# Performance work log

Hardware: AMD Instinct MI355X
Metric: run time of the kernel (lower is better)

The kernel has to match this reference:

```python
import jax, jax.numpy as jnp
import numpy as np
import math

B, S, D, H, DFF = 4, 2048, 1024, 16, 4096
DK = D // H
EPS = 1e-5

def setup_inputs() -> dict:
    key = jax.random.key(0)
    ks = jax.random.split(key, 16)
    s_d = 1.0 / math.sqrt(D)
    s_ff = 1.0 / math.sqrt(DFF)
    return {
        "x": jax.random.normal(ks[0], (B, S, D), jnp.float32),
        "wq": jax.random.uniform(ks[1], (D, D), jnp.float32, -s_d, s_d),
        "bq": jnp.zeros((D,), jnp.float32),
        "wk": jax.random.uniform(ks[2], (D, D), jnp.float32, -s_d, s_d),
        "bk": jnp.zeros((D,), jnp.float32),
        "wv": jax.random.uniform(ks[3], (D, D), jnp.float32, -s_d, s_d),
        "bv": jnp.zeros((D,), jnp.float32),
        "wo": jax.random.uniform(ks[4], (D, D), jnp.float32, -s_d, s_d),
        "bo": jnp.zeros((D,), jnp.float32),
        "w1": jax.random.uniform(ks[5], (DFF, D), jnp.float32, -s_d, s_d),
        "b1": jnp.zeros((DFF,), jnp.float32),
        "w2": jax.random.uniform(ks[6], (D, DFF), jnp.float32, -s_ff, s_ff),
        "b2": jnp.zeros((D,), jnp.float32),
        "ln1_g": jnp.ones((D,), jnp.float32),
        "ln1_b": jnp.zeros((D,), jnp.float32),
        "ln2_g": jnp.ones((D,), jnp.float32),
        "ln2_b": jnp.zeros((D,), jnp.float32),
    }

def _layernorm(x, g, b):
    mu = jnp.mean(x, axis=-1, keepdims=True)
    var = jnp.mean(jnp.square(x - mu), axis=-1, keepdims=True)
    return (x - mu) * jax.lax.rsqrt(var + EPS) * g + b

def reference(x, wq, bq, wk, bk, wv, bv, wo, bo, w1, b1, w2, b2, ln1_g, ln1_b, ln2_g, ln2_b):
    # Multi-head self-attention (dropout in eval mode -> identity).
    Q = (x @ wq.T + bq).reshape(B, S, H, DK).transpose(0, 2, 1, 3)  # (B,H,S,DK)
    K = (x @ wk.T + bk).reshape(B, S, H, DK).transpose(0, 2, 1, 3)
    V = (x @ wv.T + bv).reshape(B, S, H, DK).transpose(0, 2, 1, 3)
    scores = jnp.einsum('bhqd,bhkd->bhqk', Q, K) / math.sqrt(DK)  # (B,H,S,S)
    attn = jax.nn.softmax(scores, axis=-1)
    ctx = jnp.einsum('bhqk,bhkd->bhqd', attn, V)
    ctx = ctx.transpose(0, 2, 1, 3).reshape(B, S, D)
    attn_out = ctx @ wo.T + bo
    # SkipConnection: x + norm(sublayer)  (post-applied LayerNorm on sublayer output)
    x = x + _layernorm(attn_out, ln1_g, ln1_b)
    # FFN
    ff = jax.nn.relu(x @ w1.T + b1) @ w2.T + b2
    return x + _layernorm(ff, ln2_g, ln2_b)
```

## Files before the change

kernel.cpp:

```cpp
#include <hip/hip_runtime.h>
#include <hip/hip_bf16.h>
#include <stdint.h>


#define DI __device__ __forceinline__

typedef __attribute__((ext_vector_type(4))) float f32x4;
typedef __attribute__((ext_vector_type(16))) float f32x16;
typedef __attribute__((ext_vector_type(8))) short bf16x8;
typedef __attribute__((ext_vector_type(4))) short s16x4;

#define B_ 4
#define S_ 2048
#define D_ 1024
#define H_ 16
#define DK_ 64
#define DFF_ 4096
#define M_ 8192

DI float bf2f(short s) {
  union { unsigned u; float f; } v;
  v.u = ((unsigned)(unsigned short)s) << 16;
  return v.f;
}
DI short f2bf(float f) {
  union { float f; unsigned u; } v;
  v.f = f;
  unsigned r = v.u + 0x7FFFu + ((v.u >> 16) & 1u);
  return (short)(r >> 16);
}
DI unsigned pkbf(float lo, float hi) {
  unsigned r;
  asm("v_cvt_pk_bf16_f32 %0, %1, %2" : "=v"(r) : "v"(lo), "v"(hi));
  return r;
}
DI void plswap(unsigned& a, unsigned& b) {
  asm volatile("v_permlane32_swap_b32 %0, %1" : "+v"(a), "+v"(b));
}
DI float ex2(float x) {
  float r;
  asm("v_exp_f32 %0, %1" : "=v"(r) : "v"(x));
  return r;
}
DI float max3(float a, float b, float c) {
  float r;
  asm("v_max3_f32 %0, %1, %2, %3" : "=v"(r) : "v"(a), "v"(b), "v"(c));
  return r;
}

__global__ __launch_bounds__(256) void cvt_kernel(const float* __restrict__ in,
                                                  short* __restrict__ out, int n) {
  long i = ((long)blockIdx.x * blockDim.x + threadIdx.x) * 8;
  if (i >= n) return;
  f32x4 a = *(const f32x4*)(in + i);
  f32x4 b = *(const f32x4*)(in + i + 4);
  bf16x8 r;
  r[0] = f2bf(a[0]); r[1] = f2bf(a[1]); r[2] = f2bf(a[2]); r[3] = f2bf(a[3]);
  r[4] = f2bf(b[0]); r[5] = f2bf(b[1]); r[6] = f2bf(b[2]); r[7] = f2bf(b[3]);
  *(bf16x8*)(out + i) = r;
}

DI void gl_lds16(const void* g, void* l) {
  __builtin_amdgcn_global_load_lds(
      (const __attribute__((address_space(1))) unsigned int*)g,
      (__attribute__((address_space(3))) unsigned int*)l, 16, 0, 0);
}

#define VMCNT(N) asm volatile("s_waitcnt vmcnt(" #N ")" ::: "memory")
#define LGKM0                                          \
  asm volatile("s_waitcnt lgkmcnt(0)" ::: "memory");   \
  __builtin_amdgcn_sched_barrier(0)
#define BAR __builtin_amdgcn_s_barrier()
#define PRIO1 __builtin_amdgcn_s_setprio(1)
#define PRIO0 __builtin_amdgcn_s_setprio(0)

DI bf16x8 ldf(const short* base, int row, int kk, int lk) {
  return *(const bf16x8*)(base + row * 64 + (((4 * kk + lk) ^ (row & 7)) << 3));
}

template <int BN, int MODE>
__global__ __launch_bounds__(512, 2)
void gemm8p(const short* __restrict__ A, const short* __restrict__ Bm,
            const float* __restrict__ bias0, const float* __restrict__ bias1,
            const float* __restrict__ bias2, short* __restrict__ C,
            int M, int N, int K,
            short* __restrict__ Qo, short* __restrict__ Ko, short* __restrict__ Vo) {
  constexpr int BH = BN / 128;
  constexpr int MQ = (BN == 256 ? 4 : 2);
  constexpr int NQ = 2;
  constexpr int MF = 2 * MQ;
  constexpr int NFr = 4;
  constexpr int WM = (BN == 256 ? 128 : 64);
  constexpr int WN = 64;

  __shared__ short As[2 * 2 * 8192];
  __shared__ short Bs[2 * BH * 8192];

  const int t = threadIdx.x, w = t >> 6, l = t & 63;
  const int wm = (BN == 256 ? (w >> 2) : (w >> 1));
  const int wn = (BN == 256 ? (w & 3) : (w & 1));
  const int lr = l & 15, lk = l >> 4;
  const int ah = (BN == 256 ? wm : (wm >> 1));
  const int ab = (BN == 256 ? 0 : (wm & 1) * 64);
  const int bh = (BN == 256 ? (wn >> 1) : 0);
  const int bb = (BN == 256 ? (wn & 1) * 64 : wn * 64);

  const int gx = gridDim.x, gy = gridDim.y;
  const int orig = blockIdx.y * gx + blockIdx.x;
  const int xcd = orig & 7, k7 = orig >> 3;
  const int rw = gx >> 1, rh = gy >> 2;
  const int row0 = ((xcd >> 1) * rh + k7 / rw) * 256;
  const int col0 = ((xcd & 1) * rw + k7 % rw) * BN;

  const int NT = K >> 6;

  const int rl0 = t >> 3;
  const int csw = ((t & 7) ^ (rl0 & 7)) << 3;
  const short* Abase = A + (long)row0 * K;
  const short* Bbase = Bm + (long)col0 * K;

  auto stA = [&](int b, int kt, int h) {
    short* dst = As + ((b * 2 + h) << 13);
    const short* s = Abase + (long)(h * 128 + rl0) * K + (kt << 6) + csw;
    gl_lds16(s, dst + t * 8);
    gl_lds16(s + (long)64 * K, dst + (t + 512) * 8);
  };
  auto stB = [&](int b, int kt, int h) {
    short* dst = Bs + ((b * BH + h) << 13);
    const short* s = Bbase + (long)(h * 128 + rl0) * K + (kt << 6) + csw;
    gl_lds16(s, dst + t * 8);
    gl_lds16(s + (long)64 * K, dst + (t + 512) * 8);
  };

  f32x4 acc[MF][NFr] = {};

  stA(0, 0, 0); stA(0, 0, 1);
  stB(0, 0, 0); if (BH == 2) stB(0, 0, 1);
  stB(1, 1, 0); if (BH == 2) stB(1, 1, 1);
  stA(1, 1, 0);
  if (BH == 2) { VMCNT(6); } else { VMCNT(4); }
  BAR;

  for (int u = 0; u < NT; ++u) {
    const int rb = u & 1, ob = rb ^ 1;
    const short* aw = As + ((rb * 2 + ah) << 13);
    const short* bw = Bs + ((rb * BH + bh) << 13);
    const bool m1 = (u + 1 < NT), m2 = (u + 2 < NT);
    bf16x8 a0[MQ][2], a1[MQ][2], b0[NQ][2], b1[NQ][2];

#pragma unroll
    for (int m = 0; m < MQ; ++m) {
      const int r = ab + m * 16 + lr;
      a0[m][0] = ldf(aw, r, 0, lk); a0[m][1] = ldf(aw, r, 1, lk);
    }
#pragma unroll
    for (int n = 0; n < NQ; ++n) {
      const int r = bb + n * 16 + lr;
      b0[n][0] = ldf(bw, r, 0, lk); b0[n][1] = ldf(bw, r, 1, lk);
    }
    if (m1) stA(ob, u + 1, 1);
    BAR; LGKM0; PRIO1;
#pragma unroll
    for (int m = 0; m < MQ; ++m)
#pragma unroll
      for (int n = 0; n < NQ; ++n)
#pragma unroll
        for (int kk = 0; kk < 2; ++kk)
          acc[m][n] = __builtin_amdgcn_mfma_f32_16x16x32_bf16(
              a0[m][kk], b0[n][kk], acc[m][n], 0, 0, 0);
    PRIO0; BAR;

#pragma unroll
    for (int n = 0; n < NQ; ++n) {
      const int r = bb + (NQ + n) * 16 + lr;
      b1[n][0] = ldf(bw, r, 0, lk); b1[n][1] = ldf(bw, r, 1, lk);
    }
    BAR; LGKM0; PRIO1;
#pragma unroll
    for (int m = 0; m < MQ; ++m)
#pragma unroll
      for (int n = 0; n < NQ; ++n)
#pragma unroll
        for (int kk = 0; kk < 2; ++kk)
          acc[m][NQ + n] = __builtin_amdgcn_mfma_f32_16x16x32_bf16(
              a0[m][kk], b1[n][kk], acc[m][NQ + n], 0, 0, 0);
    PRIO0; BAR;

#pragma unroll
    for (int m = 0; m < MQ; ++m) {
      const int r = ab + (MQ + m) * 16 + lr;
      a1[m][0] = ldf(aw, r, 0, lk); a1[m][1] = ldf(aw, r, 1, lk);
    }
    if (m2) stB(rb, u + 2, 0);
    BAR; LGKM0; PRIO1;
#pragma unroll
    for (int m = 0; m < MQ; ++m)
#pragma unroll
      for (int n = 0; n < NQ; ++n)
#pragma unroll
        for (int kk = 0; kk < 2; ++kk)
          acc[MQ + m][NQ + n] = __builtin_amdgcn_mfma_f32_16x16x32_bf16(
              a1[m][kk], b1[n][kk], acc[MQ + m][NQ + n], 0, 0, 0);
    PRIO0; BAR;

    if (m2) { if (BH == 2) stB(rb, u + 2, 1); stA(rb, u + 2, 0); }
    BAR; PRIO1;
#pragma unroll
    for (int m = 0; m < MQ; ++m)
#pragma unroll
      for (int n = 0; n < NQ; ++n)
#pragma unroll
        for (int kk = 0; kk < 2; ++kk)
          acc[MQ + m][n] = __builtin_amdgcn_mfma_f32_16x16x32_bf16(
              a1[m][kk], b0[n][kk], acc[MQ + m][n], 0, 0, 0);
    PRIO0;
    if (m2) {
      if (BH == 2) { VMCNT(6); } else { VMCNT(4); }
    } else {
      VMCNT(0);
    }
    BAR;
  }

  if (MODE == 2) {
    const int which = col0 >> 10;
#pragma unroll
    for (int m = 0; m < MF; ++m) {
#pragma unroll
      for (int n = 0; n < NFr; ++n) {
        const int r0e = row0 + wm * WM + m * 16 + lk * 4;
        const int c = col0 + wn * WN + n * 16 + lr;
        const int cc = c & 1023;
        const int h = cc >> 6, dk = cc & 63;
        const int bbx = r0e >> 11, s = r0e & 2047;
        if (which == 2) {
          const float bias = bias2[cc];
          s16x4 v4;
#pragma unroll
          for (int j = 0; j < 4; ++j) v4[j] = f2bf(acc[m][n][j] + bias);
          *(s16x4*)(Vo + ((long)((bbx * H_ + h) * DK_ + dk)) * S_ + s) = v4;
        } else {
          const float bias = (which == 0 ? bias0[cc] : bias1[cc]);
          const float sc = (which == 0 ? 0.1803368801f : 1.0f);
          short* dst = (which == 0 ? Qo : Ko);
#pragma unroll
          for (int j = 0; j < 4; ++j)
            dst[(((long)(bbx * H_ + h) * S_) + s + j) * DK_ + dk] =
                f2bf((acc[m][n][j] + bias) * sc);
        }
      }
    }
  } else {
#pragma unroll
    for (int m = 0; m < MF; ++m) {
#pragma unroll
      for (int n = 0; n < NFr; ++n) {
#pragma unroll
        for (int j = 0; j < 4; ++j) {
          const int r = row0 + wm * WM + m * 16 + lk * 4 + j;
          const int c = col0 + wn * WN + n * 16 + lr;
          float v = acc[m][n][j] + bias0[c];
          if (MODE == 1) v = fmaxf(v, 0.0f);
          C[(long)r * N + c] = f2bf(v);
        }
      }
    }
  }
}

__global__ __launch_bounds__(512, 4)
void attn_kernel(const short* __restrict__ Q, const short* __restrict__ K,
                 const short* __restrict__ Vt, short* __restrict__ ctx) {
  __shared__ short Ks[2 * 4096];
  __shared__ short Vs[2 * 4096];
  const int t = threadIdx.x, w = t >> 6, l = t & 63;
  const int q31 = l & 31, hi = l >> 5;

  const int orig = blockIdx.y * gridDim.x + blockIdx.x;
  const int xcd = orig & 7, k7 = orig >> 3;
  const int bh = xcd * 8 + (k7 >> 3);
  const int q0 = (k7 & 7) * 256 + w * 32;
  const long base = (long)bh * S_ * DK_;

  bf16x8 qf[4];
  {
    const short* qp = Q + base + (long)(q0 + q31) * DK_ + hi * 8;
#pragma unroll
    for (int ks = 0; ks < 4; ++ks) qf[ks] = *(const bf16x8*)(qp + ks * 16);
  }

  bf16x8 ones;
#pragma unroll
  for (int i = 0; i < 8; ++i) ones[i] = (short)0x3F80;

  f32x16 oa[2] = {};
  f32x16 lacc = {};
  float mrun = -1e30f;

  const int trow = t >> 3;
  const int tcol = (((t & 7) ^ (trow & 7)) << 3);
  const short* Ksrc = K + base + (long)trow * DK_ + tcol;
  const short* Vsrc = Vt + base + (long)trow * S_ + tcol;

  auto stg = [&](int tile, int slot) {
    const int kb = slot * 4096;
    const int kvn = tile * 64;
    gl_lds16(Ksrc + (long)kvn * DK_, &Ks[kb + t * 8]);
    gl_lds16(Vsrc + kvn, &Vs[kb + t * 8]);
  };

  stg(0, 0);

  for (int tt = 0; tt < 32; ++tt) {
    VMCNT(0);
    BAR;
    if (tt + 1 < 32) stg(tt + 1, (tt + 1) & 1);
    const int cb = (tt & 1) * 4096;

    f32x16 sacc[2] = {};
#pragma unroll
    for (int m = 0; m < 2; ++m) {
      const int row = m * 32 + q31;
      const int sw = row & 7;
#pragma unroll
      for (int ks = 0; ks < 4; ++ks) {
        bf16x8 kf = *(const bf16x8*)&Ks[cb + row * 64 + (((2 * ks + hi) ^ sw) << 3)];
        sacc[m] = __builtin_amdgcn_mfma_f32_32x32x16_bf16(kf, qf[ks], sacc[m], 0, 0, 0);
      }
    }

    float mx[8];
#pragma unroll
    for (int r = 0; r < 8; ++r)
      mx[r] = fmaxf(max3(sacc[0][r], sacc[0][r + 8], sacc[1][r]), sacc[1][r + 8]);
    float ma = max3(mx[0], mx[1], mx[2]);
    float mb = max3(mx[3], mx[4], mx[5]);
    float tm = fmaxf(max3(mx[6], mx[7], ma), mb);
    tm = fmaxf(tm, __shfl_xor(tm, 32, 64));

    if (!__all(tm <= mrun + 8.0f)) {
      const float mnew = fmaxf(mrun, tm);
      const float fac = ex2(mrun - mnew);
#pragma unroll
      for (int r = 0; r < 16; ++r) lacc[r] *= fac;
#pragma unroll
      for (int m = 0; m < 2; ++m)
#pragma unroll
        for (int r = 0; r < 16; ++r) oa[m][r] *= fac;
      mrun = mnew;
    }

#pragma unroll
    for (int m = 0; m < 2; ++m)
#pragma unroll
      for (int r = 0; r < 16; ++r) sacc[m][r] = ex2(sacc[m][r] - mrun);

    bf16x8 pf[4];
#pragma unroll
    for (int m = 0; m < 2; ++m)
#pragma unroll
      for (int sb = 0; sb < 2; ++sb) {
        unsigned p0 = pkbf(sacc[m][8 * sb + 0], sacc[m][8 * sb + 1]);
        unsigned p1 = pkbf(sacc[m][8 * sb + 2], sacc[m][8 * sb + 3]);
        unsigned p2 = pkbf(sacc[m][8 * sb + 4], sacc[m][8 * sb + 5]);
        unsigned p3 = pkbf(sacc[m][8 * sb + 6], sacc[m][8 * sb + 7]);
        plswap(p0, p2);
        plswap(p1, p3);
        union { unsigned u[4]; bf16x8 v; } fb;
        fb.u[0] = p0; fb.u[1] = p1; fb.u[2] = p2; fb.u[3] = p3;
        pf[2 * m + sb] = fb.v;
      }

#pragma unroll
    for (int s = 0; s < 4; ++s) {
      lacc = __builtin_amdgcn_mfma_f32_32x32x16_bf16(ones, pf[s], lacc, 0, 0, 0);
#pragma unroll
      for (int mt = 0; mt < 2; ++mt) {
        const int row = mt * 32 + q31;
        const int sw = row & 7;
        bf16x8 vf = *(const bf16x8*)&Vs[cb + row * 64 + (((2 * s + hi) ^ sw) << 3)];
        oa[mt] = __builtin_amdgcn_mfma_f32_32x32x16_bf16(vf, pf[s], oa[mt], 0, 0, 0);
      }
    }
  }

  const int bb2 = bh >> 4, h = bh & 15;
  const float rl = 1.0f / lacc[0];
  short* crow = ctx + ((long)(bb2 * S_ + q0 + q31)) * D_ + h * 64 + 4 * hi;
#pragma unroll
  for (int mt = 0; mt < 2; ++mt)
#pragma unroll
    for (int g = 0; g < 4; ++g) {
      s16x4 v4;
#pragma unroll
      for (int i = 0; i < 4; ++i) v4[i] = f2bf(oa[mt][4 * g + i] * rl);
      *(s16x4*)(crow + mt * 32 + g * 8) = v4;
    }
}

template <int RES_BF16, int OUT_BF16>
__global__ __launch_bounds__(256)
void add_ln(const void* __restrict__ resv, const short* __restrict__ a,
            const float* __restrict__ gam, const float* __restrict__ bet,
            void* __restrict__ outv) {
  const int row = blockIdx.x, t = threadIdx.x;
  const int w = t >> 6, l = t & 63;
  const long roff = (long)row * D_;
  const int c = t * 4;
  s16x4 av = *(const s16x4*)(a + roff + c);
  float v0 = bf2f(av[0]), v1 = bf2f(av[1]), v2 = bf2f(av[2]), v3 = bf2f(av[3]);
  float s = v0 + v1 + v2 + v3;
#pragma unroll
  for (int mask = 1; mask < 64; mask <<= 1) s += __shfl_xor(s, mask, 64);
  __shared__ float r1[4], r2[4];
  if (l == 0) r1[w] = s;
  __syncthreads();
  float mu = (r1[0] + r1[1] + r1[2] + r1[3]) * (1.0f / D_);
  float d0 = v0 - mu, d1 = v1 - mu, d2 = v2 - mu, d3 = v3 - mu;
  float sq = d0 * d0 + d1 * d1 + d2 * d2 + d3 * d3;
#pragma unroll
  for (int mask = 1; mask < 64; mask <<= 1) sq += __shfl_xor(sq, mask, 64);
  if (l == 0) r2[w] = sq;
  __syncthreads();
  float var = (r2[0] + r2[1] + r2[2] + r2[3]) * (1.0f / D_);
  float rs = rsqrtf(var + 1e-5f);
  float res0, res1, res2, res3;
  if (RES_BF16) {
    s16x4 rv = *(const s16x4*)((const short*)resv + roff + c);
    res0 = bf2f(rv[0]); res1 = bf2f(rv[1]); res2 = bf2f(rv[2]); res3 = bf2f(rv[3]);
  } else {
    f32x4 rv = *(const f32x4*)((const float*)resv + roff + c);
    res0 = rv[0]; res1 = rv[1]; res2 = rv[2]; res3 = rv[3];
  }
  float o0 = res0 + d0 * rs * gam[c + 0] + bet[c + 0];
  float o1 = res1 + d1 * rs * gam[c + 1] + bet[c + 1];
  float o2 = res2 + d2 * rs * gam[c + 2] + bet[c + 2];
  float o3 = res3 + d3 * rs * gam[c + 3] + bet[c + 3];
  if (OUT_BF16) {
    s16x4 ov;
    ov[0] = f2bf(o0); ov[1] = f2bf(o1); ov[2] = f2bf(o2); ov[3] = f2bf(o3);
    *(s16x4*)((short*)outv + roff + c) = ov;
  } else {
    f32x4 ov;
    ov[0] = o0; ov[1] = o1; ov[2] = o2; ov[3] = o3;
    *(f32x4*)((float*)outv + roff + c) = ov;
  }
}

extern "C" void kernel_launch(void* const* d_in, const int* in_sizes, int n_in,
                              void* d_out, int out_size, void* d_ws, size_t ws_size,
                              hipStream_t stream) {
  (void)in_sizes; (void)n_in; (void)out_size; (void)ws_size;
  const float* x   = (const float*)d_in[0];
  const float* wq  = (const float*)d_in[1];
  const float* bq  = (const float*)d_in[2];
  const float* wk  = (const float*)d_in[3];
  const float* bk  = (const float*)d_in[4];
  const float* wv  = (const float*)d_in[5];
  const float* bv  = (const float*)d_in[6];
  const float* wo  = (const float*)d_in[7];
  const float* bo  = (const float*)d_in[8];
  const float* w1  = (const float*)d_in[9];
  const float* b1  = (const float*)d_in[10];
  const float* w2  = (const float*)d_in[11];
  const float* b2  = (const float*)d_in[12];
  const float* g1  = (const float*)d_in[13];
  const float* be1 = (const float*)d_in[14];
  const float* g2  = (const float*)d_in[15];
  const float* be2 = (const float*)d_in[16];

  char* ws = (char*)d_ws;
  const long MB = 1 << 20;
  short* xb    = (short*)(ws + 0 * MB);
  short* wqkvb = (short*)(ws + 16 * MB);
  short* wob   = (short*)(ws + 22 * MB);
  short* w1b   = (short*)(ws + 24 * MB);
  short* w2b   = (short*)(ws + 32 * MB);
  short* Qb    = (short*)(ws + 40 * MB);
  short* Kb    = (short*)(ws + 56 * MB);
  short* Vtb   = (short*)(ws + 72 * MB);
  short* ctxb  = (short*)(ws + 88 * MB);
  short* aout  = (short*)(ws + 40 * MB);
  short* x1b   = (short*)(ws + 56 * MB);
  short* hid   = (short*)(ws + 88 * MB);
  short* ffb   = (short*)(ws + 72 * MB);

  auto cvt = [&](const float* in, short* out, long n) {
    cvt_kernel<<<dim3((unsigned)((n / 8 + 255) / 256)), dim3(256), 0, stream>>>(in, out, (int)n);
  };
  cvt(x, xb, (long)M_ * D_);
  cvt(wq, wqkvb + 0L * D_ * D_, (long)D_ * D_);
  cvt(wk, wqkvb + 1L * D_ * D_, (long)D_ * D_);
  cvt(wv, wqkvb + 2L * D_ * D_, (long)D_ * D_);
  cvt(wo, wob, (long)D_ * D_);
  cvt(w1, w1b, (long)DFF_ * D_);
  cvt(w2, w2b, (long)D_ * DFF_);

  gemm8p<256, 2><<<dim3(3072 / 256, M_ / 256), 512, 0, stream>>>(
      xb, wqkvb, bq, bk, bv, nullptr, M_, 3072, D_, Qb, Kb, Vtb);

  attn_kernel<<<dim3(S_ / 256, B_ * H_), 512, 0, stream>>>(Qb, Kb, Vtb, ctxb);

  gemm8p<128, 0><<<dim3(D_ / 128, M_ / 256), 512, 0, stream>>>(
      ctxb, wob, bo, nullptr, nullptr, aout, M_, D_, D_, nullptr, nullptr, nullptr);

  add_ln<0, 1><<<dim3(M_), 256, 0, stream>>>(x, aout, g1, be1, x1b);

  gemm8p<256, 1><<<dim3(DFF_ / 256, M_ / 256), 512, 0, stream>>>(
      x1b, w1b, b1, nullptr, nullptr, hid, M_, DFF_, D_, nullptr, nullptr, nullptr);
  gemm8p<128, 0><<<dim3(D_ / 128, M_ / 256), 512, 0, stream>>>(
      hid, w2b, b2, nullptr, nullptr, ffb, M_, D_, DFF_, nullptr, nullptr, nullptr);

  add_ln<1, 0><<<dim3(M_), 256, 0, stream>>>(x1b, ffb, g2, be2, d_out);
}
```

Baseline: 389.6 us.

## Add dedicated simpler pipelined main loop for BN=128 GEMM tiles

Splits the GEMM main loop by tile width. The BN=256 path keeps the existing four-phase interleaved schedule. The BN=128 path gets its own loop: it loads all fragments at once, issues the global-to-LDS prefetch for tile u+2 right after one barrier, then runs a single 4x4 MFMA block. This drops the extra barriers and phase splitting for the narrower tile, with the risk of less overlap between LDS reads and MFMA issue.

```diff
diff --git a/kernel.cpp b/kernel.cpp
--- a/kernel.cpp
+++ b/kernel.cpp
@@ -134,92 +134,128 @@
 
   f32x4 acc[MF][NFr] = {};
 
-  stA(0, 0, 0); stA(0, 0, 1);
-  stB(0, 0, 0); if (BH == 2) stB(0, 0, 1);
-  stB(1, 1, 0); if (BH == 2) stB(1, 1, 1);
-  stA(1, 1, 0);
-  if (BH == 2) { VMCNT(6); } else { VMCNT(4); }
-  BAR;
-
-  for (int u = 0; u < NT; ++u) {
-    const int rb = u & 1, ob = rb ^ 1;
-    const short* aw = As + ((rb * 2 + ah) << 13);
-    const short* bw = Bs + ((rb * BH + bh) << 13);
-    const bool m1 = (u + 1 < NT), m2 = (u + 2 < NT);
-    bf16x8 a0[MQ][2], a1[MQ][2], b0[NQ][2], b1[NQ][2];
-
-#pragma unroll
-    for (int m = 0; m < MQ; ++m) {
-      const int r = ab + m * 16 + lr;
-      a0[m][0] = ldf(aw, r, 0, lk); a0[m][1] = ldf(aw, r, 1, lk);
-    }
-#pragma unroll
-    for (int n = 0; n < NQ; ++n) {
-      const int r = bb + n * 16 + lr;
-      b0[n][0] = ldf(bw, r, 0, lk); b0[n][1] = ldf(bw, r, 1, lk);
-    }
-    if (m1) stA(ob, u + 1, 1);
-    BAR; LGKM0; PRIO1;
-#pragma unroll
-    for (int m = 0; m < MQ; ++m)
-#pragma unroll
-      for (int n = 0; n < NQ; ++n)
-#pragma unroll
-        for (int kk = 0; kk < 2; ++kk)
-          acc[m][n] = __builtin_amdgcn_mfma_f32_16x16x32_bf16(
-              a0[m][kk], b0[n][kk], acc[m][n], 0, 0, 0);
-    PRIO0; BAR;
-
-#pragma unroll
-    for (int n = 0; n < NQ; ++n) {
-      const int r = bb + (NQ + n) * 16 + lr;
-      b1[n][0] = ldf(bw, r, 0, lk); b1[n][1] = ldf(bw, r, 1, lk);
-    }
-    BAR; LGKM0; PRIO1;
-#pragma unroll
-    for (int m = 0; m < MQ; ++m)
-#pragma unroll
-      for (int n = 0; n < NQ; ++n)
-#pragma unroll
-        for (int kk = 0; kk < 2; ++kk)
-          acc[m][NQ + n] = __builtin_amdgcn_mfma_f32_16x16x32_bf16(
-              a0[m][kk], b1[n][kk], acc[m][NQ + n], 0, 0, 0);
-    PRIO0; BAR;
-
-#pragma unroll
-    for (int m = 0; m < MQ; ++m) {
-      const int r = ab + (MQ + m) * 16 + lr;
-      a1[m][0] = ldf(aw, r, 0, lk); a1[m][1] = ldf(aw, r, 1, lk);
-    }
-    if (m2) stB(rb, u + 2, 0);
-    BAR; LGKM0; PRIO1;
-#pragma unroll
-    for (int m = 0; m < MQ; ++m)
-#pragma unroll
-      for (int n = 0; n < NQ; ++n)
-#pragma unroll
-        for (int kk = 0; kk < 2; ++kk)
-          acc[MQ + m][NQ + n] = __builtin_amdgcn_mfma_f32_16x16x32_bf16(
-              a1[m][kk], b1[n][kk], acc[MQ + m][NQ + n], 0, 0, 0);
-    PRIO0; BAR;
-
-    if (m2) { if (BH == 2) stB(rb, u + 2, 1); stA(rb, u + 2, 0); }
-    BAR; PRIO1;
-#pragma unroll
-    for (int m = 0; m < MQ; ++m)
-#pragma unroll
-      for (int n = 0; n < NQ; ++n)
-#pragma unroll
-        for (int kk = 0; kk < 2; ++kk)
-          acc[MQ + m][n] = __builtin_amdgcn_mfma_f32_16x16x32_bf16(
-              a1[m][kk], b0[n][kk], acc[MQ + m][n], 0, 0, 0);
-    PRIO0;
-    if (m2) {
-      if (BH == 2) { VMCNT(6); } else { VMCNT(4); }
-    } else {
-      VMCNT(0);
-    }
+  if constexpr (BN == 256) {
+    stA(0, 0, 0); stA(0, 0, 1);
+    stB(0, 0, 0); stB(0, 0, 1);
+    stB(1, 1, 0); stB(1, 1, 1);
+    stA(1, 1, 0);
+    VMCNT(6);
     BAR;
+
+    for (int u = 0; u < NT; ++u) {
+      const int rb = u & 1, ob = rb ^ 1;
+      const short* aw = As + ((rb * 2 + ah) << 13);
+      const short* bw = Bs + ((rb * BH + bh) << 13);
+      const bool m1 = (u + 1 < NT), m2 = (u + 2 < NT);
+      bf16x8 a0[MQ][2], a1[MQ][2], b0[NQ][2], b1[NQ][2];
+
+#pragma unroll
+      for (int m = 0; m < MQ; ++m) {
+        const int r = ab + m * 16 + lr;
+        a0[m][0] = ldf(aw, r, 0, lk); a0[m][1] = ldf(aw, r, 1, lk);
+      }
+#pragma unroll
+      for (int n = 0; n < NQ; ++n) {
+        const int r = bb + n * 16 + lr;
+        b0[n][0] = ldf(bw, r, 0, lk); b0[n][1] = ldf(bw, r, 1, lk);
+      }
+      if (m1) stA(ob, u + 1, 1);
+      BAR; LGKM0; PRIO1;
+#pragma unroll
+      for (int m = 0; m < MQ; ++m)
+#pragma unroll
+        for (int n = 0; n < NQ; ++n)
+#pragma unroll
+          for (int kk = 0; kk < 2; ++kk)
+            acc[m][n] = __builtin_amdgcn_mfma_f32_16x16x32_bf16(
+                a0[m][kk], b0[n][kk], acc[m][n], 0, 0, 0);
+      PRIO0; BAR;
+
+#pragma unroll
+      for (int n = 0; n < NQ; ++n) {
+        const int r = bb + (NQ + n) * 16 + lr;
+        b1[n][0] = ldf(bw, r, 0, lk); b1[n][1] = ldf(bw, r, 1, lk);
+      }
+      BAR; LGKM0; PRIO1;
+#pragma unroll
+      for (int m = 0; m < MQ; ++m)
+#pragma unroll
+        for (int n = 0; n < NQ; ++n)
+#pragma unroll
+          for (int kk = 0; kk < 2; ++kk)
+            acc[m][NQ + n] = __builtin_amdgcn_mfma_f32_16x16x32_bf16(
+                a0[m][kk], b1[n][kk], acc[m][NQ + n], 0, 0, 0);
+      PRIO0; BAR;
+
+#pragma unroll
+      for (int m = 0; m < MQ; ++m) {
+        const int r = ab + (MQ + m) * 16 + lr;
+        a1[m][0] = ldf(aw, r, 0, lk); a1[m][1] = ldf(aw, r, 1, lk);
+      }
+      if (m2) stB(rb, u + 2, 0);
+      BAR; LGKM0; PRIO1;
+#pragma unroll
+      for (int m = 0; m < MQ; ++m)
+#pragma unroll
+        for (int n = 0; n < NQ; ++n)
+#pragma unroll
+          for (int kk = 0; kk < 2; ++kk)
+            acc[MQ + m][NQ + n] = __builtin_amdgcn_mfma_f32_16x16x32_bf16(
+                a1[m][kk], b1[n][kk], acc[MQ + m][NQ + n], 0, 0, 0);
+      PRIO0; BAR;
+
+      if (m2) { stB(rb, u + 2, 1); stA(rb, u + 2, 0); }
+      BAR; PRIO1;
+#pragma unroll
+      for (int m = 0; m < MQ; ++m)
+#pragma unroll
+        for (int n = 0; n < NQ; ++n)
+#pragma unroll
+          for (int kk = 0; kk < 2; ++kk)
+            acc[MQ + m][n] = __builtin_amdgcn_mfma_f32_16x16x32_bf16(
+                a1[m][kk], b0[n][kk], acc[MQ + m][n], 0, 0, 0);
+      PRIO0;
+      if (m2) { VMCNT(6); } else { VMCNT(0); }
+      BAR;
+    }
+  } else {
+    stA(0, 0, 0); stA(0, 0, 1); stB(0, 0, 0);
+    stA(1, 1, 0); stA(1, 1, 1); stB(1, 1, 0);
+    VMCNT(6);
+    BAR;
+
+    for (int u = 0; u < NT; ++u) {
+      const int rb = u & 1;
+      const short* aw = As + ((rb * 2 + ah) << 13);
+      const short* bw = Bs + (rb << 13);
+      const bool m2 = (u + 2 < NT);
+      bf16x8 af[4][2], bfv[4][2];
+#pragma unroll
+      for (int m = 0; m < 4; ++m) {
+        const int r = ab + m * 16 + lr;
+        af[m][0] = ldf(aw, r, 0, lk); af[m][1] = ldf(aw, r, 1, lk);
+      }
+#pragma unroll
+      for (int n = 0; n < 4; ++n) {
+        const int r = bb + n * 16 + lr;
+        bfv[n][0] = ldf(bw, r, 0, lk); bfv[n][1] = ldf(bw, r, 1, lk);
+      }
+      BAR;
+      if (m2) { stA(rb, u + 2, 0); stA(rb, u + 2, 1); stB(rb, u + 2, 0); }
+      LGKM0;
+      PRIO1;
+#pragma unroll
+      for (int m = 0; m < 4; ++m)
+#pragma unroll
+        for (int n = 0; n < 4; ++n)
+#pragma unroll
+          for (int kk = 0; kk < 2; ++kk)
+            acc[m][n] = __builtin_amdgcn_mfma_f32_16x16x32_bf16(
+                af[m][kk], bfv[n][kk], acc[m][n], 0, 0, 0);
+      PRIO0;
+      if (m2) { VMCNT(6); } else { VMCNT(0); }
+      BAR;
+    }
   }
 
   if (MODE == 2) {
```

New measurement: 383.2 us. About the same (-1.7%).
